# Performance work log

Hardware: AMD Instinct MI355X
Metric: run time of the kernel (lower is better)

Reference implementation:

```python
import jax, jax.numpy as jnp
import numpy as np

MODEL_DIM = 1024
NUM_HEADS = 16
HEAD_DIM = MODEL_DIM // NUM_HEADS


def setup_inputs() -> dict:
    key = jax.random.key(0)
    ks = jax.random.split(key, 9)
    s = 1.0 / np.sqrt(MODEL_DIM)
    d = {
        "query": jax.random.normal(ks[0], (2, 2048, MODEL_DIM), dtype=jnp.float32),
        "Wq": jax.random.normal(ks[1], (MODEL_DIM, MODEL_DIM), dtype=jnp.float32) * s,
        "bq": jnp.zeros((MODEL_DIM,), dtype=jnp.float32),
        "Wk": jax.random.normal(ks[2], (MODEL_DIM, MODEL_DIM), dtype=jnp.float32) * s,
        "bk": jnp.zeros((MODEL_DIM,), dtype=jnp.float32),
        "Wv": jax.random.normal(ks[3], (MODEL_DIM, MODEL_DIM), dtype=jnp.float32) * s,
        "bv": jnp.zeros((MODEL_DIM,), dtype=jnp.float32),
        "Wo": jax.random.normal(ks[4], (MODEL_DIM, MODEL_DIM), dtype=jnp.float32) * s,
        "bo": jnp.zeros((MODEL_DIM,), dtype=jnp.float32),
    }
    return d


def reference(query, Wq, bq, Wk, bk, Wv, bv, Wo, bo):
    B, S, D = query.shape
    H, hd = NUM_HEADS, HEAD_DIM
    # self-attention: key = value = query
    q = (query @ Wq.T + bq).reshape(B, S, H, hd).transpose(0, 2, 1, 3)  # [B,H,S,hd]
    k = (query @ Wk.T + bk).reshape(B, S, H, hd).transpose(0, 2, 1, 3)
    v = (query @ Wv.T + bv).reshape(B, S, H, hd).transpose(0, 2, 1, 3)
    scores = jnp.einsum("bhqd,bhkd->bhqk", q, k) / np.sqrt(hd)  # [B,H,S,S]
    attn = jax.nn.softmax(scores, axis=-1)
    ctx = jnp.einsum("bhqk,bhkd->bhqd", attn, v)  # [B,H,S,hd]
    ctx = ctx.transpose(0, 2, 1, 3).reshape(B, S, D)
    return ctx @ Wo.T + bo
```

## Files before the change

kernel.cpp:

```cpp
#include <hip/hip_runtime.h>

typedef __attribute__((ext_vector_type(8))) __bf16 bf16x8;
typedef __attribute__((ext_vector_type(8))) unsigned short ushort8;
typedef __attribute__((ext_vector_type(4))) unsigned short ushort4v;
typedef __attribute__((ext_vector_type(4))) float f32x4;
typedef __attribute__((ext_vector_type(2))) _Float16 f16x2;
typedef __attribute__((ext_vector_type(4))) _Float16 f16x4;
typedef __attribute__((ext_vector_type(8))) _Float16 f16x8;
typedef __attribute__((ext_vector_type(2))) __fp16 fp16v2;

__device__ __forceinline__ unsigned short f2bf(float f) {
    union { float f; unsigned int u; } c; c.f = f;
    unsigned int u = c.u;
    u += 0x7fffu + ((u >> 16) & 1u);
    return (unsigned short)(u >> 16);
}

__device__ __forceinline__ void async16(const void* g, void* l) {
    __builtin_amdgcn_global_load_lds(
        (const __attribute__((address_space(1))) unsigned int*)g,
        (__attribute__((address_space(3))) unsigned int*)l, 16, 0, 0);
}

__global__ __launch_bounds__(256) void cvt_all(
    const float* __restrict__ q,  const float* __restrict__ wq,
    const float* __restrict__ wk, const float* __restrict__ wv,
    const float* __restrict__ wo,
    unsigned short* __restrict__ q_bf, unsigned short* __restrict__ wqkv,
    unsigned short* __restrict__ wo_bf, float scale_k)
{
    const int NQ = 4096 * 1024, NW = 1024 * 1024;
    int i = (blockIdx.x * 256 + threadIdx.x) * 4;
    const float* src; unsigned short* dst; float sc = 1.0f; int off;
    if (i < NQ)               { src = q;  dst = q_bf;          off = i; }
    else if (i < NQ + NW)     { src = wq; dst = wqkv;          off = i - NQ; }
    else if (i < NQ + 2 * NW) { src = wk; dst = wqkv + NW;     off = i - NQ - NW; sc = scale_k; }
    else if (i < NQ + 3 * NW) { src = wv; dst = wqkv + 2 * NW; off = i - NQ - 2 * NW; }
    else                      { src = wo; dst = wo_bf;         off = i - NQ - 3 * NW; }
    float4 v = *(const float4*)(src + off);
    ushort4v o;
    o[0] = f2bf(v.x * sc); o[1] = f2bf(v.y * sc);
    o[2] = f2bf(v.z * sc); o[3] = f2bf(v.w * sc);
    *(ushort4v*)(dst + off) = o;
}

__global__ __launch_bounds__(256) void qkv_gemm(
    const unsigned short* __restrict__ A,
    const unsigned short* __restrict__ B,
    unsigned short* __restrict__ qkv,
    _Float16* __restrict__ vtg,
    const float* __restrict__ b0, const float* __restrict__ b1, const float* __restrict__ b2,
    float s1)
{
    __shared__ __align__(16) unsigned short As[128 * 64];
    __shared__ __align__(16) unsigned short Bs[128 * 64];

    const int tid  = threadIdx.x;
    const int lane = tid & 63, wave = tid >> 6;
    const int quad = lane >> 4, l15 = lane & 15;
    const int wm = wave >> 1, wn = wave & 1;
    const int by = blockIdx.y, bx = blockIdx.x;
    const int K = 1024;

    const int srow = lane >> 3;
    const int sp   = lane & 7;
    const int scl  = sp ^ srow;
    const int sw   = l15 & 7;

    f32x4 acc[4][4];
#pragma unroll
    for (int i = 0; i < 4; ++i)
#pragma unroll
        for (int j = 0; j < 4; ++j) acc[i][j] = (f32x4)(0.0f);

    for (int kt = 0; kt < 16; ++kt) {
        __syncthreads();
#pragma unroll
        for (int j = 0; j < 4; ++j) {
            int r0 = wave * 32 + j * 8;
            async16(A + (size_t)(by * 128 + r0 + srow) * K + kt * 64 + scl * 8, &As[r0 * 64]);
            async16(B + (size_t)(bx * 128 + r0 + srow) * K + kt * 64 + scl * 8, &Bs[r0 * 64]);
        }
        __syncthreads();

#pragma unroll
        for (int kh = 0; kh < 2; ++kh) {
            bf16x8 af[4], bfr[4];
#pragma unroll
            for (int mi = 0; mi < 4; ++mi)
                af[mi] = __builtin_bit_cast(bf16x8,
                    *(const ushort8*)&As[(wm * 64 + mi * 16 + l15) * 64 + ((kh * 4 + quad) ^ sw) * 8]);
#pragma unroll
            for (int ni = 0; ni < 4; ++ni)
                bfr[ni] = __builtin_bit_cast(bf16x8,
                    *(const ushort8*)&Bs[(wn * 64 + ni * 16 + l15) * 64 + ((kh * 4 + quad) ^ sw) * 8]);
#pragma unroll
            for (int mi = 0; mi < 4; ++mi)
#pragma unroll
                for (int ni = 0; ni < 4; ++ni)
                    acc[mi][ni] = __builtin_amdgcn_mfma_f32_16x16x32_bf16(af[mi], bfr[ni], acc[mi][ni], 0, 0, 0);
        }
    }

    if (bx < 16) {
#pragma unroll
        for (int ni = 0; ni < 4; ++ni) {
            int n = bx * 128 + wn * 64 + ni * 16 + l15;
            float bias = (n < 1024) ? b0[n] : b1[n - 1024] * s1;
#pragma unroll
            for (int mi = 0; mi < 4; ++mi) {
#pragma unroll
                for (int r = 0; r < 4; ++r) {
                    int m = by * 128 + wm * 64 + mi * 16 + quad * 4 + r;
                    qkv[(size_t)m * 2048 + n] = f2bf(acc[mi][ni][r] + bias);
                }
            }
        }
    } else {
        const int mb = by * 128 + wm * 64;
        const int b  = mb >> 11;
        const int st = (mb & 2047) >> 6;
#pragma unroll
        for (int ni = 0; ni < 4; ++ni) {
            int vf = (bx - 16) * 128 + wn * 64 + ni * 16 + l15;
            int h = vf >> 6, hd = vf & 63;
            float bias = b2[vf];
            _Float16* vrow = vtg + ((size_t)((b * 16 + h) * 64 + hd)) * 2048 + st * 64;
#pragma unroll
            for (int mi = 0; mi < 4; ++mi) {
                int p = ((mi >> 1) * 4 + quad) ^ (l15 & 7);
                f16x4 o;
#pragma unroll
                for (int r = 0; r < 4; ++r) o[r] = (_Float16)(acc[mi][ni][r] + bias);
                *(f16x4*)(vrow + p * 8 + (mi & 1) * 4) = o;
            }
        }
    }
}

__global__ __launch_bounds__(256) void out_gemm(
    const unsigned short* __restrict__ A,
    const unsigned short* __restrict__ B,
    float* __restrict__ Cout,
    const float* __restrict__ bo)
{
    __shared__ __align__(16) unsigned short As[128 * 64];
    __shared__ __align__(16) unsigned short Bs[64 * 64];

    const int tid  = threadIdx.x;
    const int lane = tid & 63, wave = tid >> 6;
    const int quad = lane >> 4, l15 = lane & 15;
    const int wm = wave >> 1, wn = wave & 1;
    const int by = blockIdx.y, bx = blockIdx.x;
    const int K = 1024;

    const int srow = lane >> 3;
    const int sp   = lane & 7;
    const int scl  = sp ^ srow;
    const int sw   = l15 & 7;

    f32x4 acc[4][2];
#pragma unroll
    for (int i = 0; i < 4; ++i)
#pragma unroll
        for (int j = 0; j < 2; ++j) acc[i][j] = (f32x4)(0.0f);

    for (int kt = 0; kt < 16; ++kt) {
        __syncthreads();
#pragma unroll
        for (int j = 0; j < 4; ++j) {
            int r0 = wave * 32 + j * 8;
            async16(A + (size_t)(by * 128 + r0 + srow) * K + kt * 64 + scl * 8, &As[r0 * 64]);
        }
#pragma unroll
        for (int j = 0; j < 2; ++j) {
            int r0 = wave * 16 + j * 8;
            async16(B + (size_t)(bx * 64 + r0 + srow) * K + kt * 64 + scl * 8, &Bs[r0 * 64]);
        }
        __syncthreads();

#pragma unroll
        for (int kh = 0; kh < 2; ++kh) {
            bf16x8 af[4], bfr[2];
#pragma unroll
            for (int mi = 0; mi < 4; ++mi)
                af[mi] = __builtin_bit_cast(bf16x8,
                    *(const ushort8*)&As[(wm * 64 + mi * 16 + l15) * 64 + ((kh * 4 + quad) ^ sw) * 8]);
#pragma unroll
            for (int ni = 0; ni < 2; ++ni)
                bfr[ni] = __builtin_bit_cast(bf16x8,
                    *(const ushort8*)&Bs[(wn * 32 + ni * 16 + l15) * 64 + ((kh * 4 + quad) ^ sw) * 8]);
#pragma unroll
            for (int mi = 0; mi < 4; ++mi)
#pragma unroll
                for (int ni = 0; ni < 2; ++ni)
                    acc[mi][ni] = __builtin_amdgcn_mfma_f32_16x16x32_bf16(af[mi], bfr[ni], acc[mi][ni], 0, 0, 0);
        }
    }

#pragma unroll
    for (int ni = 0; ni < 2; ++ni) {
        int n = bx * 64 + wn * 32 + ni * 16 + l15;
        float bias = bo[n];
#pragma unroll
        for (int mi = 0; mi < 4; ++mi) {
#pragma unroll
            for (int r = 0; r < 4; ++r) {
                int m = by * 128 + wm * 64 + mi * 16 + quad * 4 + r;
                Cout[(size_t)m * 1024 + n] = acc[mi][ni][r] + bias;
            }
        }
    }
}

__global__ __launch_bounds__(256) void attn(const unsigned short* __restrict__ qkv,
                                            const _Float16* __restrict__ vtg,
                                            unsigned short* __restrict__ ctx)
{
    __shared__ __align__(16) unsigned short Ks[64 * 64];
    __shared__ __align__(16) _Float16 Vt[64 * 64];

    const int tid  = threadIdx.x;
    const int lane = tid & 63, wave = tid >> 6;
    const int quad = lane >> 4, l15 = lane & 15;
    const int bh = blockIdx.y;
    const int b = bh >> 4, h = bh & 15;
    const int q0 = blockIdx.x * 64;

    const int srow = lane >> 3;
    const int sp   = lane & 7;
    const int scl  = sp ^ srow;
    const int sw   = l15 & 7;

    bf16x8 qf[2];
    {
        int qrow = b * 2048 + q0 + wave * 16 + l15;
#pragma unroll
        for (int kh = 0; kh < 2; ++kh)
            qf[kh] = __builtin_bit_cast(bf16x8,
                *(const ushort8*)(qkv + (size_t)qrow * 2048 + h * 64 + kh * 32 + quad * 8));
    }

    f32x4 ot[4];
#pragma unroll
    for (int ht = 0; ht < 4; ++ht) ot[ht] = (f32x4)(0.0f);
    float l_acc = 0.0f;
    const fp16v2 ones = {(__fp16)1.0f, (__fp16)1.0f};

    for (int kt = 0; kt < 32; ++kt) {
        __syncthreads();
#pragma unroll
        for (int i = 0; i < 2; ++i) {
            int row = i * 32 + wave * 8 + srow;
            async16(qkv + (size_t)(b * 2048 + kt * 64 + row) * 2048 + 1024 + h * 64 + scl * 8,
                    &Ks[(i * 32 + wave * 8) * 64]);
            async16(vtg + (size_t)(bh * 64 + row) * 2048 + kt * 64 + sp * 8,
                    (unsigned short*)&Vt[(i * 32 + wave * 8) * 64]);
        }
        __syncthreads();

        f16x4 pv[4];
#pragma unroll
        for (int mt = 0; mt < 4; ++mt) {
            const unsigned short* kb = &Ks[(mt * 16 + l15) * 64];
            bf16x8 k0 = __builtin_bit_cast(bf16x8, *(const ushort8*)(kb + (quad ^ sw) * 8));
            bf16x8 k1 = __builtin_bit_cast(bf16x8, *(const ushort8*)(kb + ((quad ^ sw) ^ 4) * 8));
            f32x4 s4 = (f32x4)(0.0f);
            s4 = __builtin_amdgcn_mfma_f32_16x16x32_bf16(k0, qf[0], s4, 0, 0, 0);
            s4 = __builtin_amdgcn_mfma_f32_16x16x32_bf16(k1, qf[1], s4, 0, 0, 0);
            float p0 = __builtin_amdgcn_exp2f(s4[0]);
            float p1 = __builtin_amdgcn_exp2f(s4[1]);
            float p2 = __builtin_amdgcn_exp2f(s4[2]);
            float p3 = __builtin_amdgcn_exp2f(s4[3]);
            fp16v2 lo = __builtin_amdgcn_cvt_pkrtz(p0, p1);
            fp16v2 hi = __builtin_amdgcn_cvt_pkrtz(p2, p3);
            l_acc = __builtin_amdgcn_fdot2(lo, ones, l_acc, false);
            l_acc = __builtin_amdgcn_fdot2(hi, ones, l_acc, false);
            f16x2 lo2 = __builtin_bit_cast(f16x2, lo);
            f16x2 hi2 = __builtin_bit_cast(f16x2, hi);
            pv[mt] = __builtin_shufflevector(lo2, hi2, 0, 1, 2, 3);
        }

#pragma unroll
        for (int ht = 0; ht < 4; ++ht) {
            const _Float16* vb = &Vt[(ht * 16 + l15) * 64];
#pragma unroll
            for (int g = 0; g < 2; ++g) {
                f16x8 v8 = *(const f16x8*)(vb + (((g * 4 + quad) ^ sw)) * 8);
                f16x4 vlo = __builtin_shufflevector(v8, v8, 0, 1, 2, 3);
                f16x4 vhi = __builtin_shufflevector(v8, v8, 4, 5, 6, 7);
                ot[ht] = __builtin_amdgcn_mfma_f32_16x16x16f16(vlo, pv[2 * g],     ot[ht], 0, 0, 0);
                ot[ht] = __builtin_amdgcn_mfma_f32_16x16x16f16(vhi, pv[2 * g + 1], ot[ht], 0, 0, 0);
            }
        }
    }

    {
        float l = l_acc;
        l += __shfl_xor(l, 16, 64);
        l += __shfl_xor(l, 32, 64);
        float inv = 1.0f / l;
        int qrow = b * 2048 + q0 + wave * 16 + l15;
#pragma unroll
        for (int ht = 0; ht < 4; ++ht) {
            ushort4v o4;
#pragma unroll
            for (int r = 0; r < 4; ++r) o4[r] = f2bf(ot[ht][r] * inv);
            *(ushort4v*)(ctx + (size_t)qrow * 1024 + h * 64 + ht * 16 + quad * 4) = o4;
        }
    }
}

extern "C" void kernel_launch(void* const* d_in, const int* in_sizes, int n_in,
                              void* d_out, int out_size, void* d_ws, size_t ws_size,
                              hipStream_t stream) {
    const float* query = (const float*)d_in[0];
    const float* Wq = (const float*)d_in[1];
    const float* bq = (const float*)d_in[2];
    const float* Wk = (const float*)d_in[3];
    const float* bk = (const float*)d_in[4];
    const float* Wv = (const float*)d_in[5];
    const float* bv = (const float*)d_in[6];
    const float* Wo = (const float*)d_in[7];
    const float* bo = (const float*)d_in[8];

    char* ws = (char*)d_ws;
    unsigned short* q_bf  = (unsigned short*)(ws);
    unsigned short* ctx   = (unsigned short*)(ws);
    unsigned short* wqkv  = (unsigned short*)(ws + 8388608);
    unsigned short* wo_bf = (unsigned short*)(ws + 14680064);
    unsigned short* qkv   = (unsigned short*)(ws + 16777216);
    _Float16*       vtg   = (_Float16*)(ws + 33554432);

    const float SCALE = 0.125f * 1.4426950408889634f;

    cvt_all<<<8192, 256, 0, stream>>>(query, Wq, Wk, Wv, Wo, q_bf, wqkv, wo_bf, SCALE);
    qkv_gemm<<<dim3(24, 32), 256, 0, stream>>>(q_bf, wqkv, qkv, vtg, bq, bk, bv, SCALE);
    attn<<<dim3(32, 32), 256, 0, stream>>>(qkv, vtg, ctx);
    out_gemm<<<dim3(16, 32), 256, 0, stream>>>(ctx, wo_bf, (float*)d_out, bo);
}
```

Before: 202.4 us.

## Load two KV tiles per sync, use 16x16x32 f16 MFMA, fp32 row sums

New measurement: 199.4 us. No clear change (-1.5%).

```diff
diff --git a/kernel.cpp b/kernel.cpp
--- a/kernel.cpp
+++ b/kernel.cpp
@@ -213,12 +213,12 @@
     }
 }
 
-__global__ __launch_bounds__(256) void attn(const unsigned short* __restrict__ qkv,
-                                            const _Float16* __restrict__ vtg,
-                                            unsigned short* __restrict__ ctx)
+__global__ __launch_bounds__(256, 4) void attn(const unsigned short* __restrict__ qkv,
+                                               const _Float16* __restrict__ vtg,
+                                               unsigned short* __restrict__ ctx)
 {
-    __shared__ __align__(16) unsigned short Ks[64 * 64];
-    __shared__ __align__(16) _Float16 Vt[64 * 64];
+    __shared__ __align__(16) unsigned short Ks[2 * 64 * 64];
+    __shared__ __align__(16) _Float16 Vt[2 * 64 * 64];
 
     const int tid  = threadIdx.x;
     const int lane = tid & 63, wave = tid >> 6;
@@ -245,52 +245,59 @@
 #pragma unroll
     for (int ht = 0; ht < 4; ++ht) ot[ht] = (f32x4)(0.0f);
     float l_acc = 0.0f;
-    const fp16v2 ones = {(__fp16)1.0f, (__fp16)1.0f};
-
-    for (int kt = 0; kt < 32; ++kt) {
-        __syncthreads();
-#pragma unroll
-        for (int i = 0; i < 2; ++i) {
-            int row = i * 32 + wave * 8 + srow;
-            async16(qkv + (size_t)(b * 2048 + kt * 64 + row) * 2048 + 1024 + h * 64 + scl * 8,
-                    &Ks[(i * 32 + wave * 8) * 64]);
-            async16(vtg + (size_t)(bh * 64 + row) * 2048 + kt * 64 + sp * 8,
-                    (unsigned short*)&Vt[(i * 32 + wave * 8) * 64]);
-        }
-        __syncthreads();
-
-        f16x4 pv[4];
-#pragma unroll
-        for (int mt = 0; mt < 4; ++mt) {
-            const unsigned short* kb = &Ks[(mt * 16 + l15) * 64];
-            bf16x8 k0 = __builtin_bit_cast(bf16x8, *(const ushort8*)(kb + (quad ^ sw) * 8));
-            bf16x8 k1 = __builtin_bit_cast(bf16x8, *(const ushort8*)(kb + ((quad ^ sw) ^ 4) * 8));
-            f32x4 s4 = (f32x4)(0.0f);
-            s4 = __builtin_amdgcn_mfma_f32_16x16x32_bf16(k0, qf[0], s4, 0, 0, 0);
-            s4 = __builtin_amdgcn_mfma_f32_16x16x32_bf16(k1, qf[1], s4, 0, 0, 0);
-            float p0 = __builtin_amdgcn_exp2f(s4[0]);
-            float p1 = __builtin_amdgcn_exp2f(s4[1]);
-            float p2 = __builtin_amdgcn_exp2f(s4[2]);
-            float p3 = __builtin_amdgcn_exp2f(s4[3]);
-            fp16v2 lo = __builtin_amdgcn_cvt_pkrtz(p0, p1);
-            fp16v2 hi = __builtin_amdgcn_cvt_pkrtz(p2, p3);
-            l_acc = __builtin_amdgcn_fdot2(lo, ones, l_acc, false);
-            l_acc = __builtin_amdgcn_fdot2(hi, ones, l_acc, false);
-            f16x2 lo2 = __builtin_bit_cast(f16x2, lo);
-            f16x2 hi2 = __builtin_bit_cast(f16x2, hi);
-            pv[mt] = __builtin_shufflevector(lo2, hi2, 0, 1, 2, 3);
-        }
-
-#pragma unroll
-        for (int ht = 0; ht < 4; ++ht) {
-            const _Float16* vb = &Vt[(ht * 16 + l15) * 64];
-#pragma unroll
-            for (int g = 0; g < 2; ++g) {
-                f16x8 v8 = *(const f16x8*)(vb + (((g * 4 + quad) ^ sw)) * 8);
-                f16x4 vlo = __builtin_shufflevector(v8, v8, 0, 1, 2, 3);
-                f16x4 vhi = __builtin_shufflevector(v8, v8, 4, 5, 6, 7);
-                ot[ht] = __builtin_amdgcn_mfma_f32_16x16x16f16(vlo, pv[2 * g],     ot[ht], 0, 0, 0);
-                ot[ht] = __builtin_amdgcn_mfma_f32_16x16x16f16(vhi, pv[2 * g + 1], ot[ht], 0, 0, 0);
+
+    for (int KT = 0; KT < 16; ++KT) {
+        __syncthreads();
+#pragma unroll
+        for (int j = 0; j < 2; ++j) {
+            int kt = KT * 2 + j;
+#pragma unroll
+            for (int i = 0; i < 2; ++i) {
+                int row = i * 32 + wave * 8 + srow;
+                async16(qkv + (size_t)(b * 2048 + kt * 64 + row) * 2048 + 1024 + h * 64 + scl * 8,
+                        &Ks[j * 4096 + (i * 32 + wave * 8) * 64]);
+                async16(vtg + (size_t)(bh * 64 + row) * 2048 + kt * 64 + sp * 8,
+                        (unsigned short*)&Vt[j * 4096 + (i * 32 + wave * 8) * 64]);
+            }
+        }
+        __syncthreads();
+
+#pragma unroll
+        for (int j = 0; j < 2; ++j) {
+            const unsigned short* KsJ = &Ks[j * 4096];
+            const _Float16*       VtJ = &Vt[j * 4096];
+
+            f16x4 pv[4];
+#pragma unroll
+            for (int mt = 0; mt < 4; ++mt) {
+                const unsigned short* kb = &KsJ[(mt * 16 + l15) * 64];
+                bf16x8 k0 = __builtin_bit_cast(bf16x8, *(const ushort8*)(kb + (quad ^ sw) * 8));
+                bf16x8 k1 = __builtin_bit_cast(bf16x8, *(const ushort8*)(kb + ((quad ^ sw) ^ 4) * 8));
+                f32x4 s4 = (f32x4)(0.0f);
+                s4 = __builtin_amdgcn_mfma_f32_16x16x32_bf16(k0, qf[0], s4, 0, 0, 0);
+                s4 = __builtin_amdgcn_mfma_f32_16x16x32_bf16(k1, qf[1], s4, 0, 0, 0);
+                float p0 = __builtin_amdgcn_exp2f(s4[0]);
+                float p1 = __builtin_amdgcn_exp2f(s4[1]);
+                float p2 = __builtin_amdgcn_exp2f(s4[2]);
+                float p3 = __builtin_amdgcn_exp2f(s4[3]);
+                fp16v2 lo = __builtin_amdgcn_cvt_pkrtz(p0, p1);
+                fp16v2 hi = __builtin_amdgcn_cvt_pkrtz(p2, p3);
+                l_acc += (p0 + p1) + (p2 + p3);
+                f16x2 lo2 = __builtin_bit_cast(f16x2, lo);
+                f16x2 hi2 = __builtin_bit_cast(f16x2, hi);
+                pv[mt] = __builtin_shufflevector(lo2, hi2, 0, 1, 2, 3);
+            }
+
+#pragma unroll
+            for (int ht = 0; ht < 4; ++ht) {
+                const _Float16* vb = &VtJ[(ht * 16 + l15) * 64];
+#pragma unroll
+                for (int g = 0; g < 2; ++g) {
+                    f16x8 v8 = *(const f16x8*)(vb + (((g * 4 + quad) ^ sw)) * 8);
+                    f16x8 p8 = __builtin_shufflevector(pv[2 * g], pv[2 * g + 1],
+                                                       0, 1, 2, 3, 4, 5, 6, 7);
+                    ot[ht] = __builtin_amdgcn_mfma_f32_16x16x32_f16(v8, p8, ot[ht], 0, 0, 0);
+                }
             }
         }
     }
```
